# Performance work log

Measured on AMD Instinct MI355X. Metric: run time of the kernel, lower is better.

The kernel has to match this reference:

```python
import jax, jax.numpy as jnp
import numpy as np

D_MODEL = 1024
D_STATE = 16
D_CONV = 4
EXPAND = 2
D_INNER = D_MODEL * EXPAND
DT_RANK = max(D_MODEL // 16, 1)  # 64
B, L = 2, 2048


def setup_inputs() -> dict:
    key = jax.random.key(0)
    ks = jax.random.split(key, 10)
    s = lambda fan_in: 1.0 / np.sqrt(fan_in)
    x = jax.random.normal(ks[0], (B, L, D_MODEL), dtype=jnp.float32)
    ln_w = jnp.ones((D_MODEL,), jnp.float32)
    ln_b = jnp.zeros((D_MODEL,), jnp.float32)
    in_proj_w = jax.random.normal(ks[1], (D_MODEL, 2 * D_INNER), jnp.float32) * s(D_MODEL)
    conv_w = jax.random.normal(ks[2], (D_INNER, D_CONV), jnp.float32) * s(D_CONV)
    conv_b = jnp.zeros((D_INNER,), jnp.float32)
    x_proj_w = jax.random.normal(ks[3], (D_INNER, DT_RANK + 2 * D_STATE), jnp.float32) * s(D_INNER)
    dt_proj_w = jax.random.normal(ks[4], (DT_RANK, D_INNER), jnp.float32) * s(DT_RANK)
    dt_proj_b = jax.random.normal(ks[5], (D_INNER,), jnp.float32) * 0.1
    # A_log init: log(arange(1, d_state+1)) broadcast over d_inner
    A_log = jnp.broadcast_to(jnp.log(jnp.arange(1, D_STATE + 1, dtype=jnp.float32))[None, :], (D_INNER, D_STATE)).copy()
    D_param = jnp.ones((D_INNER,), jnp.float32)
    out_proj_w = jax.random.normal(ks[6], (D_INNER, D_MODEL), jnp.float32) * s(D_INNER)
    res_scale = jnp.ones((1,), jnp.float32)
    return dict(x=x, ln_w=ln_w, ln_b=ln_b, in_proj_w=in_proj_w, conv_w=conv_w,
                conv_b=conv_b, x_proj_w=x_proj_w, dt_proj_w=dt_proj_w,
                dt_proj_b=dt_proj_b, A_log=A_log, D_param=D_param,
                out_proj_w=out_proj_w, res_scale=res_scale)


def _layernorm(x, w, b, eps=1e-5):
    mu = jnp.mean(x, axis=-1, keepdims=True)
    var = jnp.mean(jnp.square(x - mu), axis=-1, keepdims=True)
    return (x - mu) * jax.lax.rsqrt(var + eps) * w + b


def _causal_depthwise_conv1d(x_cl, conv_w, conv_b):
    # x_cl: [B, C, L]; conv_w: [C, K] depthwise; causal left-pad K-1
    out = jax.lax.conv_general_dilated(
        x_cl, conv_w[:, None, :],  # kernel [C,1,K]
        window_strides=(1,), padding=[(D_CONV - 1, 0)],
        dimension_numbers=('NCH', 'OIH', 'NCH'),
        feature_group_count=D_INNER)
    return out + conv_b[None, :, None]


def reference(x, ln_w, ln_b, in_proj_w, conv_w, conv_b, x_proj_w, dt_proj_w,
              dt_proj_b, A_log, D_param, out_proj_w, res_scale):
    residual = x
    xn = _layernorm(x, ln_w, ln_b)                       # [B,L,D]
    xz = xn @ in_proj_w                                  # [B,L,2*Di]
    x_main, z = jnp.split(xz, 2, axis=-1)                # each [B,L,Di]
    x_conv = _causal_depthwise_conv1d(jnp.swapaxes(x_main, 1, 2), conv_w, conv_b)
    new_conv_state = jnp.swapaxes(x_main, 1, 2)[:, :, -(D_CONV - 1):]
    x_main = jax.nn.silu(jnp.swapaxes(x_conv, 1, 2))     # [B,L,Di]

    A = -jnp.exp(A_log)                                  # [Di,N]
    x_dbl = x_main @ x_proj_w                            # [B,L,dt_rank+2N]
    dt, B_ssm, C_ssm = jnp.split(x_dbl, [DT_RANK, DT_RANK + D_STATE], axis=-1)
    dt = jax.nn.softplus(dt @ dt_proj_w + dt_proj_b)     # [B,L,Di]
    dA = jnp.exp(A[None, None] * dt[..., None])          # [B,L,Di,N]
    dBx = dt[..., None] * B_ssm[:, :, None, :] * x_main[..., None]  # [B,L,Di,N]

    def scan_fn(h, inp):
        dA_t, dBx_t, C_t = inp                           # [B,Di,N],[B,Di,N],[B,N]
        h = dA_t * h + dBx_t
        y_t = jnp.einsum('bdn,bn->bd', h, C_t)
        return h, y_t

    h0 = jnp.zeros((x.shape[0], D_INNER, D_STATE), x.dtype)
    new_ssm_state, ys = jax.lax.scan(
        scan_fn, h0,
        (jnp.swapaxes(dA, 0, 1), jnp.swapaxes(dBx, 0, 1), jnp.swapaxes(C_ssm, 0, 1)))
    y = jnp.swapaxes(ys, 0, 1)                           # [B,L,Di]
    y = y + x_main * D_param[None, None, :]
    y = y * jax.nn.silu(z)
    out = res_scale * (y @ out_proj_w) + residual        # [B,L,D]
    return out, new_ssm_state, new_conv_state
```

## Files before the change

### kernel.cpp

```cpp
#include <hip/hip_runtime.h>
#include <math.h>

#define D_MODEL 1024
#define D_STATE 16
#define D_CONVK 4
#define D_INNER 2048
#define DT_RANK 64
#define BB 2
#define LL 2048
#define NROWS (BB*LL)
#define NC 128
#define CH (LL/NC)
#define XZLD 4096
#define LOG2E 1.44269504088896340736f
#define LN2   0.69314718055994530942f

typedef __attribute__((ext_vector_type(8))) short bf16x8;
typedef __attribute__((ext_vector_type(8))) unsigned short u16x8;
typedef __attribute__((ext_vector_type(4))) float f32x4;

typedef __attribute__((address_space(3))) unsigned char lds_ucp;
typedef const __attribute__((address_space(1))) unsigned char glb_ucp;
#define GLD16(gp, lp) __builtin_amdgcn_global_load_lds((glb_ucp*)(gp), (lds_ucp*)(lp), 16, 0, 0)

__device__ inline unsigned short f2bf(float f) {
    union { float f; unsigned u; } c; c.f = f;
    unsigned r = c.u + 0x7fff + ((c.u >> 16) & 1);
    return (unsigned short)(r >> 16);
}
__device__ inline float bf2f(unsigned short s) {
    union { unsigned u; float f; } c; c.u = ((unsigned)s) << 16;
    return c.f;
}
__device__ inline float fexp2(float x) { return __builtin_amdgcn_exp2f(x); }
__device__ inline float frcp(float x)  { return __builtin_amdgcn_rcpf(x); }
__device__ inline float fsilu(float x) { return x * frcp(1.0f + fexp2(-x * LOG2E)); }

__global__ __launch_bounds__(256)
void prologue_kernel(const float* __restrict__ x, const float* __restrict__ lw,
                     const float* __restrict__ lb, unsigned short* __restrict__ xnb,
                     const float* __restrict__ Win, const float* __restrict__ Wout,
                     const float* __restrict__ Wx, const float* __restrict__ Wdt,
                     unsigned short* __restrict__ wtin, unsigned short* __restrict__ wtout,
                     unsigned short* __restrict__ Wxt, unsigned short* __restrict__ Wdtt) {
    if (blockIdx.x < NROWS) {
        int row = blockIdx.x;
        const float* xr = x + (size_t)row * D_MODEL;
        float4 v = ((const float4*)xr)[threadIdx.x];
        float s  = v.x + v.y + v.z + v.w;
        float ss = v.x*v.x + v.y*v.y + v.z*v.z + v.w*v.w;
        for (int off = 32; off > 0; off >>= 1) {
            s  += __shfl_down(s, off);
            ss += __shfl_down(ss, off);
        }
        __shared__ float red[8];
        int lane = threadIdx.x & 63, wv = threadIdx.x >> 6;
        if (lane == 0) { red[wv] = s; red[wv + 4] = ss; }
        __syncthreads();
        if (threadIdx.x == 0) {
            float ts  = red[0] + red[1] + red[2] + red[3];
            float tss = red[4] + red[5] + red[6] + red[7];
            float mu  = ts / D_MODEL;
            float var = tss / D_MODEL - mu * mu;
            red[0] = mu; red[1] = rsqrtf(var + 1e-5f);
        }
        __syncthreads();
        float mu = red[0], rs = red[1];
        float4 w4 = ((const float4*)lw)[threadIdx.x];
        float4 b4 = ((const float4*)lb)[threadIdx.x];
        ushort4 o;
        o.x = f2bf((v.x - mu) * rs * w4.x + b4.x);
        o.y = f2bf((v.y - mu) * rs * w4.y + b4.y);
        o.z = f2bf((v.z - mu) * rs * w4.z + b4.z);
        o.w = f2bf((v.w - mu) * rs * w4.w + b4.w);
        ((ushort4*)(xnb + (size_t)row * D_MODEL))[threadIdx.x] = o;
        return;
    }
    int tb = blockIdx.x - NROWS;
    int bx = tb % 228, by = tb / 228;
    __shared__ float t[32][33];
    const float* W; unsigned short* Wt; int K, Nsrc, xb;
    if (bx < 128)      { W = Win;  Wt = wtin;  K = 1024; Nsrc = 4096; xb = bx; }
    else if (bx < 160) { W = Wout; Wt = wtout; K = 2048; Nsrc = 1024; xb = bx - 128; }
    else if (bx < 164) { W = Wx;   Wt = Wxt;   K = 2048; Nsrc = 96;   xb = bx - 160; }
    else               { W = Wdt;  Wt = Wdtt;  K = 64;   Nsrc = 2048; xb = bx - 164; }
    int k0 = by * 32, n0 = xb * 32;
    if (k0 >= K) return;
    int tx = threadIdx.x & 31, ty = threadIdx.x >> 5;
#pragma unroll
    for (int i = 0; i < 32; i += 8)
        t[ty + i][tx] = (n0 + tx < Nsrc)
            ? W[(size_t)(k0 + ty + i) * Nsrc + n0 + tx] : 0.0f;
    __syncthreads();
#pragma unroll
    for (int i = 0; i < 32; i += 8)
        Wt[(size_t)(n0 + ty + i) * K + k0 + tx] = f2bf(t[tx][ty + i]);
}

__global__ __launch_bounds__(512)
void mfma_gemm_big(const unsigned short* __restrict__ A,
                   const unsigned short* __restrict__ Wt,
                   int ldc, int K, unsigned short* __restrict__ out2) {
    __shared__ short As[256 * 64];
    __shared__ short Bs[128 * 64];
    int tid = threadIdx.x;
    int lane = tid & 63, w = tid >> 6;
    int wr2 = w & 3, wc2 = w >> 2;
    int row0 = blockIdx.y * 256, col0 = blockIdx.x * 128;
    f32x4 acc[4][4] = {};
    const unsigned short* gA0 = A  + (size_t)row0 * K;
    const unsigned short* gB0 = Wt + (size_t)col0 * K;
    int r_in = lane >> 3;
    int e16  = (lane & 7) * 8;
    int quad = lane >> 4, r16 = lane & 15;
    for (int k0 = 0; k0 < K; k0 += 64) {
        __syncthreads();
#pragma unroll
        for (int t = 0; t < 4; ++t) {
            int p = w * 4 + t;
            int row = p * 8 + r_in;
            GLD16(gA0 + (size_t)row * K + k0 + e16, (char*)As + p * 1024);
        }
#pragma unroll
        for (int t = 0; t < 2; ++t) {
            int p = w * 2 + t;
            int row = p * 8 + r_in;
            GLD16(gB0 + (size_t)row * K + k0 + e16, (char*)Bs + p * 1024);
        }
        __syncthreads();
#pragma unroll
        for (int ks = 0; ks < 2; ++ks) {
            bf16x8 af[4], bfr[4];
#pragma unroll
            for (int i = 0; i < 4; ++i) {
                af[i]  = *(const bf16x8*)&As[(wr2 * 64 + i * 16 + r16) * 64 + ks * 32 + quad * 8];
                bfr[i] = *(const bf16x8*)&Bs[(wc2 * 64 + i * 16 + r16) * 64 + ks * 32 + quad * 8];
            }
#pragma unroll
            for (int mi = 0; mi < 4; ++mi)
#pragma unroll
                for (int ni = 0; ni < 4; ++ni)
                    acc[mi][ni] = __builtin_amdgcn_mfma_f32_16x16x32_bf16(
                        af[mi], bfr[ni], acc[mi][ni], 0, 0, 0);
        }
    }
    int odd = lane & 1;
#pragma unroll
    for (int mi = 0; mi < 4; ++mi)
#pragma unroll
        for (int ni = 0; ni < 4; ++ni) {
            int colE = col0 + wc2 * 64 + ni * 16 + r16;
#pragma unroll
            for (int rp = 0; rp < 2; ++rp) {
                int rowE = row0 + wr2 * 64 + mi * 16 + quad * 4 + rp * 2;
                int row  = rowE + odd;
                int colp = colE - odd;
                unsigned hh = (unsigned)f2bf(acc[mi][ni][rp*2]) |
                              ((unsigned)f2bf(acc[mi][ni][rp*2+1]) << 16);
                unsigned ph = __shfl_xor((int)hh, 1);
                unsigned u_even = (hh & 0xffffu) | (ph << 16);
                unsigned u_odd  = (ph >> 16) | (hh & 0xffff0000u);
                unsigned u = odd ? u_odd : u_even;
                *(unsigned*)&out2[(size_t)row * ldc + colp] = u;
            }
        }
}

__global__ __launch_bounds__(256)
void mfma_gemm(const unsigned short* __restrict__ A,
               const unsigned short* __restrict__ Wt,
               float* __restrict__ C, int ldc, int K, int kchunk,
               size_t zstride, int mode,
               const float* __restrict__ aux,
               int Ncols, unsigned short* __restrict__ out2) {
    __shared__ short As[128 * 64];
    __shared__ short Bs[128 * 64];
    int tid = threadIdx.x;
    int lane = tid & 63, w = tid >> 6;
    int wm = w & 1, wn = w >> 1;
    int row0 = blockIdx.y * 128, col0 = blockIdx.x * 128;
    int kb = blockIdx.z * kchunk, ke = kb + kchunk;
    C += (size_t)blockIdx.z * zstride;
    f32x4 acc[4][4] = {};
    const unsigned short* gA0 = A  + (size_t)row0 * K;
    const unsigned short* gB0 = Wt + (size_t)col0 * K;
    int r_in = lane >> 3;
    int e16  = (lane & 7) * 8;
    int quad = lane >> 4, r16 = lane & 15;
    for (int k0 = kb; k0 < ke; k0 += 64) {
        __syncthreads();
#pragma unroll
        for (int t = 0; t < 4; ++t) {
            int p = w * 4 + t;
            int row = p * 8 + r_in;
            GLD16(gA0 + (size_t)row * K + k0 + e16, (char*)As + p * 1024);
            GLD16(gB0 + (size_t)row * K + k0 + e16, (char*)Bs + p * 1024);
        }
        __syncthreads();
#pragma unroll
        for (int ks = 0; ks < 2; ++ks) {
            bf16x8 af[4], bfr[4];
#pragma unroll
            for (int i = 0; i < 4; ++i) {
                af[i]  = *(const bf16x8*)&As[(wm * 64 + i * 16 + r16) * 64 + ks * 32 + quad * 8];
                bfr[i] = *(const bf16x8*)&Bs[(wn * 64 + i * 16 + r16) * 64 + ks * 32 + quad * 8];
            }
#pragma unroll
            for (int mi = 0; mi < 4; ++mi)
#pragma unroll
                for (int ni = 0; ni < 4; ++ni)
                    acc[mi][ni] = __builtin_amdgcn_mfma_f32_16x16x32_bf16(
                        af[mi], bfr[ni], acc[mi][ni], 0, 0, 0);
        }
    }
    int odd = lane & 1;
#pragma unroll
    for (int mi = 0; mi < 4; ++mi)
#pragma unroll
        for (int ni = 0; ni < 4; ++ni) {
            int colE = col0 + wn * 64 + ni * 16 + r16;
            float v[4];
#pragma unroll
            for (int r = 0; r < 4; ++r) v[r] = acc[mi][ni][r];
            if (mode == 4) {
                float bv = aux[colE];
#pragma unroll
                for (int r = 0; r < 4; ++r) {
                    float tv = v[r] + bv;
                    v[r] = (tv > 20.0f) ? tv
                         : LN2 * __builtin_amdgcn_logf(1.0f + fexp2(tv * LOG2E));
                }
            }
#pragma unroll
            for (int rp = 0; rp < 2; ++rp) {
                int rowE = row0 + wm * 64 + mi * 16 + quad * 4 + rp * 2;
                int row  = rowE + odd;
                int colp = colE - odd;
                if (mode >= 3) {
                    unsigned hh = (unsigned)f2bf(v[rp*2]) | ((unsigned)f2bf(v[rp*2+1]) << 16);
                    unsigned ph = __shfl_xor((int)hh, 1);
                    unsigned u_even = (hh & 0xffffu) | (ph << 16);
                    unsigned u_odd  = (ph >> 16) | (hh & 0xffff0000u);
                    unsigned u = odd ? u_odd : u_even;
                    *(unsigned*)&out2[(size_t)row * ldc + colp] = u;
                } else {
                    float a0 = v[rp*2], a1 = v[rp*2+1];
                    float b0 = __shfl_xor(a0, 1), b1 = __shfl_xor(a1, 1);
                    float2 f2;
                    f2.x = odd ? b1 : a0;
                    f2.y = odd ? a1 : b0;
                    if (colp < Ncols)
                        *(float2*)&C[(size_t)row * ldc + colp] = f2;
                }
            }
        }
}

__global__ __launch_bounds__(256)
void xdbl_reduce(const float* __restrict__ P,
                 unsigned short* __restrict__ xdtr, float* __restrict__ xbc) {
    const int S1 = NROWS * 96;
    int t = blockIdx.x * 256 + threadIdx.x;
    float s = 0.0f;
#pragma unroll
    for (int k = 0; k < 8; ++k) s += P[t + k * S1];
    int row = t / 96, col = t - row * 96;
    if (col < DT_RANK) xdtr[(size_t)row * DT_RANK + col] = f2bf(s);
    else xbc[(size_t)row * 32 + col - DT_RANK] = s;
}

__global__ __launch_bounds__(256)
void out_final(const float* __restrict__ P0, const float* __restrict__ P1,
               const float* __restrict__ x, const float* __restrict__ rscale,
               float* __restrict__ out) {
    int t = blockIdx.x * 256 + threadIdx.x;
    float rs = rscale[0];
    float4 a = ((const float4*)P0)[t];
    float4 b = ((const float4*)P1)[t];
    float4 r = ((const float4*)x)[t];
    float4 o;
    o.x = rs * (a.x + b.x) + r.x;
    o.y = rs * (a.y + b.y) + r.y;
    o.z = rs * (a.z + b.z) + r.z;
    o.w = rs * (a.w + b.w) + r.w;
    ((float4*)out)[t] = o;
}

__global__ __launch_bounds__(256)
void conv_kernel(const unsigned short* __restrict__ xzb, const float* __restrict__ cw,
                 const float* __restrict__ cb, unsigned short* __restrict__ xs,
                 float* __restrict__ conv_state_out) {
    int loct = blockIdx.x & 255;
    int b    = blockIdx.x >> 8;
    int d0   = threadIdx.x * 8;
    float wgt[8][4];
#pragma unroll
    for (int j = 0; j < 8; ++j) {
        float4 w4 = *(const float4*)(cw + (size_t)(d0 + j) * 4);
        wgt[j][0] = w4.x; wgt[j][1] = w4.y; wgt[j][2] = w4.z; wgt[j][3] = w4.w;
    }
    float bias[8];
    *(float4*)&bias[0] = *(const float4*)(cb + d0);
    *(float4*)&bias[4] = *(const float4*)(cb + d0 + 4);
    float xr[11][8];
#pragma unroll
    for (int r = 0; r < 11; ++r) {
        int l = loct * 8 - 3 + r;
        if (l >= 0) {
            u16x8 v = *(const u16x8*)&xzb[((size_t)b * LL + l) * XZLD + d0];
#pragma unroll
            for (int j = 0; j < 8; ++j) xr[r][j] = bf2f(v[j]);
        } else {
#pragma unroll
            for (int j = 0; j < 8; ++j) xr[r][j] = 0.0f;
        }
    }
#pragma unroll
    for (int i = 0; i < 8; ++i) {
        unsigned short o[8];
#pragma unroll
        for (int j = 0; j < 8; ++j) {
            float a = bias[j];
#pragma unroll
            for (int k = 0; k < 4; ++k) a = fmaf(xr[i + k][j], wgt[j][k], a);
            o[j] = f2bf(fsilu(a));
        }
        *(u16x8*)&xs[((size_t)b * LL + loct * 8 + i) * D_INNER + d0] = *(u16x8*)o;
    }
    if (loct == 255) {
#pragma unroll
        for (int i = 8; i < 11; ++i)
#pragma unroll
            for (int j = 0; j < 8; ++j)
                conv_state_out[((size_t)b * D_INNER + d0 + j) * 3 + (i - 8)] = xr[i][j];
    }
}

__global__ __launch_bounds__(256)
void scan_part1(const unsigned short* __restrict__ dt, const float* __restrict__ xbc,
                const unsigned short* __restrict__ xs,
                const float* __restrict__ A_log,
                float* __restrict__ Sbuf, float* __restrict__ Tbuf) {
    __shared__ float Bs[CH][32];
    int d = blockIdx.x * 256 + threadIdx.x;
    int c = blockIdx.y, b = blockIdx.z;
    size_t rowbase = (size_t)b * LL + (size_t)c * CH;
    for (int e = threadIdx.x; e < CH * 32; e += 256) {
        int i = e >> 5, j = e & 31;
        Bs[i][j] = xbc[(rowbase + i) * 32 + j];
    }
    float al2[16];
    {
        const float4* ap = (const float4*)(A_log + (size_t)d * D_STATE);
#pragma unroll
        for (int q = 0; q < 4; ++q) {
            float4 a4 = ap[q];
            al2[q*4+0] = -fexp2(a4.x * LOG2E) * LOG2E;
            al2[q*4+1] = -fexp2(a4.y * LOG2E) * LOG2E;
            al2[q*4+2] = -fexp2(a4.z * LOG2E) * LOG2E;
            al2[q*4+3] = -fexp2(a4.w * LOG2E) * LOG2E;
        }
    }
    __syncthreads();
    float S[16];
#pragma unroll
    for (int n = 0; n < 16; ++n) S[n] = 0.0f;
    float Tsum = 0.0f;
    float dtv = bf2f(dt[rowbase * D_INNER + d]);
    float xv  = bf2f(xs[rowbase * D_INNER + d]);
    for (int i = 0; i < CH; ++i) {
        float dtn = 0.0f, xn2 = 0.0f;
        if (i + 1 < CH) {
            size_t r2 = (rowbase + i + 1) * D_INNER + d;
            dtn = bf2f(dt[r2]); xn2 = bf2f(xs[r2]);
        }
        Tsum += dtv;
        float dtx = dtv * xv;
#pragma unroll
        for (int q = 0; q < 4; ++q) {
            float4 Bv = *(const float4*)&Bs[i][q * 4];
            S[q*4+0] = fmaf(fexp2(al2[q*4+0] * dtv), S[q*4+0], dtx * Bv.x);
            S[q*4+1] = fmaf(fexp2(al2[q*4+1] * dtv), S[q*4+1], dtx * Bv.y);
            S[q*4+2] = fmaf(fexp2(al2[q*4+2] * dtv), S[q*4+2], dtx * Bv.z);
            S[q*4+3] = fmaf(fexp2(al2[q*4+3] * dtv), S[q*4+3], dtx * Bv.w);
        }
        dtv = dtn; xv = xn2;
    }
    size_t o = (((size_t)b * NC + c) * D_INNER + d) * D_STATE;
#pragma unroll
    for (int q = 0; q < 4; ++q) {
        float4 Sv;
        Sv.x = S[q*4+0]; Sv.y = S[q*4+1]; Sv.z = S[q*4+2]; Sv.w = S[q*4+3];
        *(float4*)(Sbuf + o + q * 4) = Sv;
    }
    Tbuf[((size_t)b * NC + c) * D_INNER + d] = Tsum;
}

__global__ __launch_bounds__(256)
void scan_part2(const float* __restrict__ S, const float* __restrict__ Tbuf,
                const float* __restrict__ A_log, float* __restrict__ Hin) {
    int t = blockIdx.x * 256 + threadIdx.x;
    int b = t >> 15;
    int rem = t & 32767;
    int d = rem >> 4;
    float al2 = -fexp2(A_log[rem] * LOG2E) * LOG2E;
    size_t sbase = (size_t)b * NC * (D_INNER * D_STATE) + rem;
    size_t tbase = (size_t)b * NC * D_INNER + d;
    float h = 0.0f;
    for (int c = 0; c < NC; ++c) {
        size_t sq = sbase + (size_t)c * (D_INNER * D_STATE);
        float s = S[sq];
        float T = Tbuf[tbase + (size_t)c * D_INNER];
        Hin[sq] = h;
        h = fmaf(fexp2(al2 * T), h, s);
    }
}

__global__ __launch_bounds__(256)
void scan_part3(const unsigned short* __restrict__ dt, const float* __restrict__ xbc,
                const unsigned short* __restrict__ xs,
                const unsigned short* __restrict__ xzb,
                const float* __restrict__ A_log, const float* __restrict__ Dp,
                const float* __restrict__ Hin,
                unsigned short* __restrict__ y, float* __restrict__ ssm_out) {
    __shared__ float Bs[CH][32];
    int d = blockIdx.x * 256 + threadIdx.x;
    int c = blockIdx.y, b = blockIdx.z;
    size_t rowbase = (size_t)b * LL + (size_t)c * CH;
    for (int e = threadIdx.x; e < CH * 32; e += 256) {
        int i = e >> 5, j = e & 31;
        Bs[i][j] = xbc[(rowbase + i) * 32 + j];
    }
    float al2[16];
    {
        const float4* ap = (const float4*)(A_log + (size_t)d * D_STATE);
#pragma unroll
        for (int q = 0; q < 4; ++q) {
            float4 a4 = ap[q];
            al2[q*4+0] = -fexp2(a4.x * LOG2E) * LOG2E;
            al2[q*4+1] = -fexp2(a4.y * LOG2E) * LOG2E;
            al2[q*4+2] = -fexp2(a4.z * LOG2E) * LOG2E;
            al2[q*4+3] = -fexp2(a4.w * LOG2E) * LOG2E;
        }
    }
    float Dv = Dp[d];
    float h[16];
    {
        const float4* hp = (const float4*)(Hin + (((size_t)b * NC + c) * D_INNER + d) * D_STATE);
#pragma unroll
        for (int q = 0; q < 4; ++q) {
            float4 h4 = hp[q];
            h[q*4+0] = h4.x; h[q*4+1] = h4.y; h[q*4+2] = h4.z; h[q*4+3] = h4.w;
        }
    }
    __syncthreads();
    size_t r0 = rowbase * D_INNER + d;
    float dtv = bf2f(dt[r0]);
    float xv  = bf2f(xs[r0]);
    float zv  = bf2f(xzb[rowbase * XZLD + D_INNER + d]);
    for (int i = 0; i < CH; ++i) {
        float dtn = 0.0f, xn2 = 0.0f, zn2 = 0.0f;
        if (i + 1 < CH) {
            size_t r2 = (rowbase + i + 1) * D_INNER + d;
            dtn = bf2f(dt[r2]); xn2 = bf2f(xs[r2]);
            zn2 = bf2f(xzb[(rowbase + i + 1) * XZLD + D_INNER + d]);
        }
        float dtx = dtv * xv;
        float yv = 0.0f;
#pragma unroll
        for (int q = 0; q < 4; ++q) {
            float4 Bv = *(const float4*)&Bs[i][q * 4];
            float4 Cv = *(const float4*)&Bs[i][16 + q * 4];
            h[q*4+0] = fmaf(fexp2(al2[q*4+0] * dtv), h[q*4+0], dtx * Bv.x);
            h[q*4+1] = fmaf(fexp2(al2[q*4+1] * dtv), h[q*4+1], dtx * Bv.y);
            h[q*4+2] = fmaf(fexp2(al2[q*4+2] * dtv), h[q*4+2], dtx * Bv.z);
            h[q*4+3] = fmaf(fexp2(al2[q*4+3] * dtv), h[q*4+3], dtx * Bv.w);
            yv = fmaf(h[q*4+0], Cv.x, yv);
            yv = fmaf(h[q*4+1], Cv.y, yv);
            yv = fmaf(h[q*4+2], Cv.z, yv);
            yv = fmaf(h[q*4+3], Cv.w, yv);
        }
        yv = (yv + xv * Dv) * fsilu(zv);
        y[(rowbase + i) * D_INNER + d] = f2bf(yv);
        dtv = dtn; xv = xn2; zv = zn2;
    }
    if (c == NC - 1) {
        float* sp = ssm_out + ((size_t)b * D_INNER + d) * D_STATE;
#pragma unroll
        for (int q = 0; q < 4; ++q) {
            float4 h4;
            h4.x = h[q*4+0]; h4.y = h[q*4+1]; h4.z = h[q*4+2]; h4.w = h[q*4+3];
            *(float4*)(sp + q * 4) = h4;
        }
    }
}

extern "C" void kernel_launch(void* const* d_in, const int* in_sizes, int n_in,
                              void* d_out, int out_size, void* d_ws, size_t ws_size,
                              hipStream_t stream) {
    (void)in_sizes; (void)n_in; (void)out_size; (void)ws_size;
    const float* x      = (const float*)d_in[0];
    const float* ln_w   = (const float*)d_in[1];
    const float* ln_b   = (const float*)d_in[2];
    const float* Win    = (const float*)d_in[3];
    const float* convw  = (const float*)d_in[4];
    const float* convb  = (const float*)d_in[5];
    const float* Wx     = (const float*)d_in[6];
    const float* Wdt    = (const float*)d_in[7];
    const float* bdt    = (const float*)d_in[8];
    const float* A_log  = (const float*)d_in[9];
    const float* Dp     = (const float*)d_in[10];
    const float* Wout   = (const float*)d_in[11];
    const float* rscale = (const float*)d_in[12];

    float* out      = (float*)d_out;
    float* ssm_out  = out + (size_t)NROWS * D_MODEL;
    float* conv_out = ssm_out + (size_t)BB * D_INNER * D_STATE;

    float* ws = (float*)d_ws;
    unsigned short* xzb = (unsigned short*)ws;
    unsigned short* xsb = xzb + (size_t)NROWS * XZLD;
    unsigned short* dtbb = xsb + (size_t)NROWS * D_INNER;
    float* xbc  = (float*)(dtbb + (size_t)NROWS * D_INNER);
    unsigned short* xdtr = (unsigned short*)(xbc + (size_t)NROWS * 32);
    unsigned short* xnb  = xdtr + (size_t)NROWS * DT_RANK;
    unsigned short* wtin = xnb + (size_t)NROWS * D_MODEL;
    unsigned short* wtout = wtin + (size_t)(2 * D_INNER) * D_MODEL;
    unsigned short* Wxt  = wtout + (size_t)D_MODEL * D_INNER;
    unsigned short* Wdtt = Wxt + (size_t)128 * D_INNER;
    float* Tbuf = (float*)(Wdtt + (size_t)D_INNER * DT_RANK);
    float* Sbuf = Tbuf + (size_t)BB * NC * D_INNER;
    float* Pxdbl = Sbuf;
    float* Hin   = Sbuf;
    float* P0 = Sbuf;
    float* P1 = Sbuf + (size_t)NROWS * D_MODEL;
    unsigned short* ybuf = xnb;

    prologue_kernel<<<NROWS + 228 * 64, 256, 0, stream>>>(
        x, ln_w, ln_b, xnb, Win, Wout, Wx, Wdt, wtin, wtout, Wxt, Wdtt);

    mfma_gemm_big<<<dim3(2 * D_INNER / 128, NROWS / 256), 512, 0, stream>>>(
        xnb, wtin, XZLD, D_MODEL, xzb);

    conv_kernel<<<BB * (LL / 8), 256, 0, stream>>>(
        xzb, convw, convb, xsb, conv_out);

    mfma_gemm<<<dim3(1, NROWS / 128, 8), 256, 0, stream>>>(
        xsb, Wxt, Pxdbl, 96, D_INNER, D_INNER / 8, (size_t)NROWS * 96, 0,
        nullptr, 96, nullptr);
    xdbl_reduce<<<(NROWS * 96) / 256, 256, 0, stream>>>(Pxdbl, xdtr, xbc);

    mfma_gemm<<<dim3(D_INNER / 128, NROWS / 128), 256, 0, stream>>>(
        xdtr, Wdtt, nullptr, D_INNER, DT_RANK, DT_RANK, 0, 4,
        bdt, D_INNER, dtbb);

    scan_part1<<<dim3(D_INNER / 256, NC, BB), 256, 0, stream>>>(
        dtbb, xbc, xsb, A_log, Sbuf, Tbuf);
    scan_part2<<<(BB * D_INNER * D_STATE) / 256, 256, 0, stream>>>(
        Sbuf, Tbuf, A_log, Hin);
    scan_part3<<<dim3(D_INNER / 256, NC, BB), 256, 0, stream>>>(
        dtbb, xbc, xsb, xzb, A_log, Dp, Hin, ybuf, ssm_out);

    mfma_gemm<<<dim3(D_MODEL / 128, NROWS / 128, 2), 256, 0, stream>>>(
        ybuf, wtout, P0, D_MODEL, D_INNER, D_INNER / 2,
        (size_t)NROWS * D_MODEL, 0,
        nullptr, D_MODEL, nullptr);

    out_final<<<(NROWS * D_MODEL) / (256 * 4), 256, 0, stream>>>(
        P0, P1, x, rscale, out);
}
```

Baseline: 303.8 us.

## Rewrite in_proj GEMM with 4-stage async LDS pipeline, 256x256 tiles, swizzle

Replaces the in_proj GEMM with a version that uses 256x256 output tiles and a 4-buffer ring of BK=32 LDS tiles filled by global_load_lds. Manual vmcnt waits let loads for three tiles ahead overlap MFMA compute, and a single barrier per iteration replaces the two syncs. It also XOR-swizzles the LDS layout to avoid bank conflicts, remaps block IDs so neighbouring blocks share L2 data, and raises MFMA priority with setprio. In exchange it holds a larger per-warp accumulator (8x4 fragments) that raises register pressure, and the grid shrinks to 256 blocks.

```diff
diff --git a/kernel.cpp b/kernel.cpp
--- a/kernel.cpp
+++ b/kernel.cpp
@@ -97,62 +97,75 @@
         Wt[(size_t)(n0 + ty + i) * K + k0 + tx] = f2bf(t[tx][ty + i]);
 }
 
-__global__ __launch_bounds__(512)
-void mfma_gemm_big(const unsigned short* __restrict__ A,
-                   const unsigned short* __restrict__ Wt,
-                   int ldc, int K, unsigned short* __restrict__ out2) {
-    __shared__ short As[256 * 64];
-    __shared__ short Bs[128 * 64];
+__global__ __launch_bounds__(512, 2)
+void mfma_gemm_pipe(const unsigned short* __restrict__ A,
+                    const unsigned short* __restrict__ Wt,
+                    int ldc, int K, unsigned short* __restrict__ out2) {
+    __shared__ short As[4][256 * 32];
+    __shared__ short Bs[4][256 * 32];
     int tid = threadIdx.x;
     int lane = tid & 63, w = tid >> 6;
-    int wr2 = w & 3, wc2 = w >> 2;
-    int row0 = blockIdx.y * 256, col0 = blockIdx.x * 128;
-    f32x4 acc[4][4] = {};
+    int wm = w & 1, wn = w >> 1;
+    int bid = blockIdx.y * gridDim.x + blockIdx.x;
+    int cpx = (gridDim.x * gridDim.y) >> 3;
+    int swz = (bid & 7) * cpx + (bid >> 3);
+    int bx = swz % gridDim.x, by = swz / gridDim.x;
+    int row0 = by * 256, col0 = bx * 256;
     const unsigned short* gA0 = A  + (size_t)row0 * K;
     const unsigned short* gB0 = Wt + (size_t)col0 * K;
-    int r_in = lane >> 3;
-    int e16  = (lane & 7) * 8;
+    int rowin = lane >> 2;
+    int e8    = (((lane & 3) ^ (rowin & 3)) * 8);
     int quad = lane >> 4, r16 = lane & 15;
-    for (int k0 = 0; k0 < K; k0 += 64) {
-        __syncthreads();
-#pragma unroll
-        for (int t = 0; t < 4; ++t) {
-            int p = w * 4 + t;
-            int row = p * 8 + r_in;
-            GLD16(gA0 + (size_t)row * K + k0 + e16, (char*)As + p * 1024);
-        }
-#pragma unroll
-        for (int t = 0; t < 2; ++t) {
-            int p = w * 2 + t;
-            int row = p * 8 + r_in;
-            GLD16(gB0 + (size_t)row * K + k0 + e16, (char*)Bs + p * 1024);
-        }
-        __syncthreads();
-#pragma unroll
-        for (int ks = 0; ks < 2; ++ks) {
-            bf16x8 af[4], bfr[4];
-#pragma unroll
-            for (int i = 0; i < 4; ++i) {
-                af[i]  = *(const bf16x8*)&As[(wr2 * 64 + i * 16 + r16) * 64 + ks * 32 + quad * 8];
-                bfr[i] = *(const bf16x8*)&Bs[(wc2 * 64 + i * 16 + r16) * 64 + ks * 32 + quad * 8];
-            }
-#pragma unroll
-            for (int mi = 0; mi < 4; ++mi)
-#pragma unroll
-                for (int ni = 0; ni < 4; ++ni)
-                    acc[mi][ni] = __builtin_amdgcn_mfma_f32_16x16x32_bf16(
-                        af[mi], bfr[ni], acc[mi][ni], 0, 0, 0);
-        }
-    }
+    int cslot = (quad ^ (r16 & 3)) * 8;
+    f32x4 acc[8][4] = {};
+    int nt = K >> 5;
+
+#define STAGE_TILE(tt) do {                                                    \
+    int _b = (tt) & 3; int _k0 = (tt) << 5;                                    \
+    _Pragma("unroll")                                                          \
+    for (int _r = 0; _r < 2; ++_r) {                                           \
+        int _p = _r * 8 + w;                                                   \
+        int _grow = _p * 16 + rowin;                                           \
+        GLD16(gA0 + (size_t)_grow * K + _k0 + e8, (char*)&As[_b][0] + _p * 1024); \
+        GLD16(gB0 + (size_t)_grow * K + _k0 + e8, (char*)&Bs[_b][0] + _p * 1024); \
+    } } while (0)
+
+    STAGE_TILE(0); STAGE_TILE(1); STAGE_TILE(2);
+    for (int t = 0; t < nt; ++t) {
+        if (t < nt - 2)       asm volatile("s_waitcnt vmcnt(8)" ::: "memory");
+        else if (t == nt - 2) asm volatile("s_waitcnt vmcnt(4)" ::: "memory");
+        else                  asm volatile("s_waitcnt vmcnt(0)" ::: "memory");
+        __builtin_amdgcn_s_barrier();
+        __builtin_amdgcn_sched_barrier(0);
+        if (t + 3 < nt) STAGE_TILE(t + 3);
+        const short* Ab = &As[t & 3][0];
+        const short* Bb = &Bs[t & 3][0];
+        bf16x8 bfr[4], af[8];
+#pragma unroll
+        for (int i = 0; i < 4; ++i)
+            bfr[i] = *(const bf16x8*)&Bb[(wn * 64 + i * 16 + r16) * 32 + cslot];
+#pragma unroll
+        for (int i = 0; i < 8; ++i)
+            af[i] = *(const bf16x8*)&Ab[(wm * 128 + i * 16 + r16) * 32 + cslot];
+        __builtin_amdgcn_s_setprio(1);
+#pragma unroll
+        for (int mi = 0; mi < 8; ++mi)
+#pragma unroll
+            for (int ni = 0; ni < 4; ++ni)
+                acc[mi][ni] = __builtin_amdgcn_mfma_f32_16x16x32_bf16(
+                    af[mi], bfr[ni], acc[mi][ni], 0, 0, 0);
+        __builtin_amdgcn_s_setprio(0);
+    }
+#undef STAGE_TILE
     int odd = lane & 1;
 #pragma unroll
-    for (int mi = 0; mi < 4; ++mi)
+    for (int mi = 0; mi < 8; ++mi)
 #pragma unroll
         for (int ni = 0; ni < 4; ++ni) {
-            int colE = col0 + wc2 * 64 + ni * 16 + r16;
+            int colE = col0 + wn * 64 + ni * 16 + r16;
 #pragma unroll
             for (int rp = 0; rp < 2; ++rp) {
-                int rowE = row0 + wr2 * 64 + mi * 16 + quad * 4 + rp * 2;
+                int rowE = row0 + wm * 128 + mi * 16 + quad * 4 + rp * 2;
                 int row  = rowE + odd;
                 int colp = colE - odd;
                 unsigned hh = (unsigned)f2bf(acc[mi][ni][rp*2]) |
@@ -539,7 +552,7 @@
     prologue_kernel<<<NROWS + 228 * 64, 256, 0, stream>>>(
         x, ln_w, ln_b, xnb, Win, Wout, Wx, Wdt, wtin, wtout, Wxt, Wdtt);
 
-    mfma_gemm_big<<<dim3(2 * D_INNER / 128, NROWS / 256), 512, 0, stream>>>(
+    mfma_gemm_pipe<<<dim3(2 * D_INNER / 256, NROWS / 256), 512, 0, stream>>>(
         xnb, wtin, XZLD, D_MODEL, xzb);
 
     conv_kernel<<<BB * (LL / 8), 256, 0, stream>>>(
```

Result: slower. 310.3 us (+2.2%).
